# Kernel tuning notes

Hardware: AMD Instinct MI355X
Metric: run time of the kernel (lower is better)

The kernel has to match this reference:

```python
import jax, jax.numpy as jnp
import numpy as np

N_NODES = 10000
N_EDGES = 100000
C = 64          # in_channels == out_channels (required by x_i + x_m)
D_EDGE = 16     # edge_attr feature dim


def setup_inputs() -> dict:
    key = jax.random.key(0)
    k_x, k_ei, k_ea, k_w, k_b, k_r, k_bias = jax.random.split(key, 7)
    x = jax.random.normal(k_x, (N_NODES, C), dtype=jnp.float32)
    edge_index = jax.random.randint(k_ei, (2, N_EDGES), 0, N_NODES, dtype=jnp.int32)
    edge_attr = jax.random.normal(k_ea, (N_EDGES, D_EDGE), dtype=jnp.float32)
    # nn = Linear(D_EDGE -> C*C), producing per-edge [C, C] weight matrices
    W_nn = jax.random.normal(k_w, (D_EDGE, C * C), dtype=jnp.float32) * (1.0 / np.sqrt(D_EDGE))
    b_nn = jax.random.normal(k_b, (C * C,), dtype=jnp.float32) * 0.01
    root = jax.random.normal(k_r, (C, C), dtype=jnp.float32) * (1.0 / np.sqrt(C))
    bias = jax.random.normal(k_bias, (C,), dtype=jnp.float32) * 0.01
    return {"x": x, "edge_index": edge_index, "edge_attr": edge_attr,
            "W_nn": W_nn, "b_nn": b_nn, "root": root, "bias": bias}


def reference(x, edge_index, edge_attr, W_nn, b_nn, root, bias):
    N, Cc = x.shape
    row, col = edge_index[0], edge_index[1]
    # per-edge weight matrices from nn(edge_attr): [E, C, C]
    e = (edge_attr @ W_nn + b_nn).reshape(-1, Cc, Cc)
    # gather source features and apply edge-conditioned matmul: [E, C]
    m = jnp.einsum('ec,eco->eo', x[row], e)
    # Faithful to torch loop: x_m[i] = m[col == i].mean() -> SCALAR mean over
    # all elements of incoming messages, broadcast across the feature row.
    seg_sum = jax.ops.segment_sum(m.sum(axis=1), col, num_segments=N)       # [N]
    cnt = jax.ops.segment_sum(jnp.ones_like(col, dtype=x.dtype), col,
                              num_segments=N) * Cc                            # [N]
    mean = jnp.where(cnt > 0, seg_sum / jnp.maximum(cnt, 1.0), 0.0)          # [N]
    x_m = jnp.broadcast_to(mean[:, None], (N, Cc))                            # [N, C]
    # root transform + bias
    out = x @ root + bias + x_m
    return out
```

## Files before the change

### kernel.cpp

```cpp
#include <hip/hip_runtime.h>
#include <hip/hip_bf16.h>


#define CC 64
#define DE 16
#define PAD 65

__global__ __launch_bounds__(256) void k_node(const float* __restrict__ W,
                                              const float* __restrict__ b,
                                              const float* __restrict__ x,
                                              float* __restrict__ g,
                                              float* __restrict__ h,
                                              float* __restrict__ zreg,
                                              int zcount, int N) {
    __shared__ float ws[1024 + CC];
    int tid = threadIdx.x;

    for (int i = blockIdx.x * 256 + tid; i < zcount; i += gridDim.x * 256)
        zreg[i] = 0.f;

    for (int p = tid; p < 1024 + CC; p += 256) {
        const float4* src = (p < 1024) ? (const float4*)(W + (size_t)p * CC)
                                       : (const float4*)(b + (size_t)(p - 1024) * CC);
        float s = 0.f;
#pragma unroll
        for (int i = 0; i < 16; ++i) { float4 v = src[i]; s += v.x + v.y + v.z + v.w; }
        ws[p] = s;
    }
    __syncthreads();

    int n = blockIdx.x * 256 + tid;
    if (n >= N) return;

    const float4* x4  = (const float4*)(x + (size_t)n * CC);
    const float4* ws4 = (const float4*)ws;
    const float4* bs4 = (const float4*)(ws + 1024);

    float4 xr[16];
#pragma unroll
    for (int i = 0; i < 16; ++i) xr[i] = x4[i];

    float acc[DE];
#pragma unroll
    for (int d = 0; d < DE; ++d) acc[d] = 0.f;
    float hh = 0.f;

#pragma unroll
    for (int c4 = 0; c4 < 16; ++c4) {
        float4 xv = xr[c4];
        float4 bv = bs4[c4];
        hh += bv.x * xv.x + bv.y * xv.y + bv.z * xv.z + bv.w * xv.w;
#pragma unroll
        for (int d = 0; d < DE; ++d) {
            float4 wv = ws4[d * 16 + c4];
            acc[d] += wv.x * xv.x + wv.y * xv.y + wv.z * xv.z + wv.w * xv.w;
        }
    }
    float4* g4 = (float4*)(g + (size_t)n * DE);
    g4[0] = make_float4(acc[0], acc[1], acc[2], acc[3]);
    g4[1] = make_float4(acc[4], acc[5], acc[6], acc[7]);
    g4[2] = make_float4(acc[8], acc[9], acc[10], acc[11]);
    g4[3] = make_float4(acc[12], acc[13], acc[14], acc[15]);
    h[n] = hh;
}

__global__ __launch_bounds__(256) void k_edge(const int* __restrict__ ei,
                                              const float* __restrict__ ea,
                                              const float* __restrict__ g,
                                              const float* __restrict__ h,
                                              float* __restrict__ seg,
                                              float* __restrict__ cnt,
                                              int E) {
    int e = blockIdx.x * 256 + threadIdx.x;
    if (e >= E) return;
    int r  = ei[e];
    int cn = ei[E + e];
    const float4* a4 = (const float4*)(ea + (size_t)e * DE);
    const float4* g4 = (const float4*)(g + (size_t)r * DE);
    float4 a0 = a4[0], a1 = a4[1], a2 = a4[2], a3 = a4[3];
    float4 g0 = g4[0], g1 = g4[1], g2 = g4[2], g3 = g4[3];
    float s = h[r]
        + a0.x * g0.x + a0.y * g0.y + a0.z * g0.z + a0.w * g0.w
        + a1.x * g1.x + a1.y * g1.y + a1.z * g1.z + a1.w * g1.w
        + a2.x * g2.x + a2.y * g2.y + a2.z * g2.z + a2.w * g2.w
        + a3.x * g3.x + a3.y * g3.y + a3.z * g3.z + a3.w * g3.w;
    atomicAdd(seg + cn, s);
    atomicAdd(cnt + cn, 1.0f);
}

__global__ __launch_bounds__(256) void k_final(const float* __restrict__ x,
                                               const float* __restrict__ root,
                                               const float* __restrict__ bias,
                                               const float* __restrict__ seg,
                                               const float* __restrict__ cnt,
                                               float* __restrict__ out,
                                               int N) {
    __shared__ float rt[CC * CC];
    __shared__ float xs[16 * PAD];
    __shared__ float bi[CC];
    __shared__ float mn[16];
    int tid = threadIdx.x;
    int n0 = blockIdx.x * 16;

#pragma unroll
    for (int i = 0; i < 16; ++i) rt[tid + i * 256] = root[tid + i * 256];
#pragma unroll
    for (int it = 0; it < 4; ++it) {
        int i = it * 256 + tid;
        if ((size_t)n0 * CC + i < (size_t)N * CC)
            xs[(i >> 6) * PAD + (i & 63)] = x[(size_t)n0 * CC + i];
    }
    if (tid < CC) bi[tid] = bias[tid];
    if (tid < 16 && n0 + tid < N) {
        float c = cnt[n0 + tid];
        mn[tid] = c > 0.f ? seg[n0 + tid] / (c * (float)CC) : 0.f;
    }
    __syncthreads();

    int nl = tid >> 4, ci = tid & 15;
    int n = n0 + nl;
    if (n >= N) return;

    const float4* rt4 = (const float4*)rt;
    const float4* bi4 = (const float4*)bi;
    float m = mn[nl];
    float4 bv = bi4[ci];
    float4 acc = make_float4(bv.x + m, bv.y + m, bv.z + m, bv.w + m);
#pragma unroll
    for (int k = 0; k < CC; ++k) {
        float a  = xs[nl * PAD + k];
        float4 w = rt4[k * 16 + ci];
        acc.x += a * w.x; acc.y += a * w.y; acc.z += a * w.z; acc.w += a * w.w;
    }
    *(float4*)(out + (size_t)n * CC + ci * 4) = acc;
}

extern "C" void kernel_launch(void* const* d_in, const int* in_sizes, int n_in,
                              void* d_out, int out_size, void* d_ws, size_t ws_size,
                              hipStream_t stream) {
    const float* x    = (const float*)d_in[0];
    const int*   ei   = (const int*)  d_in[1];
    const float* ea   = (const float*)d_in[2];
    const float* W    = (const float*)d_in[3];
    const float* b    = (const float*)d_in[4];
    const float* root = (const float*)d_in[5];
    const float* bias = (const float*)d_in[6];
    float* out = (float*)d_out;
    float* ws  = (float*)d_ws;

    const int N = in_sizes[0] / CC;
    const int E = in_sizes[1] / 2;

    float* h    = ws;
    float* seg  = ws + N;
    float* cnt  = ws + 2 * N;
    float* g    = ws + 3 * N;

    int nBlocks = (N + 255) / 256;
    int eBlocks = (E + 255) / 256;
    int fBlocks = (N + 15) / 16;

    k_node <<<nBlocks, 256, 0, stream>>>(W, b, x, g, h, seg, 2 * N, N);
    k_edge <<<eBlocks, 256, 0, stream>>>(ei, ea, g, h, seg, cnt, E);
    k_final<<<fBlocks, 256, 0, stream>>>(x, root, bias, seg, cnt, out, N);
}
```

Baseline: 107.0 us.

## Fuse node, edge and final stages into one cooperative kernel with grid syncs

Replaces the three separate launches (node projection, edge scatter-add, root transform) with a single persistent cooperative kernel. The stages are separated by grid-wide synchronisation, and each block loops over its chunks of nodes and edges. The intent is to remove the launch gaps and tail effects between the three small kernels. In exchange it pays for two grid.sync barriers, extra host-side occupancy queries, and a persistent grid sized by occupancy. The original three-kernel path is kept as a fallback if the cooperative launch fails.

```diff
diff --git a/kernel.cpp b/kernel.cpp
--- a/kernel.cpp
+++ b/kernel.cpp
@@ -1,10 +1,133 @@
 #include <hip/hip_runtime.h>
+#include <hip/hip_cooperative_groups.h>
 #include <hip/hip_bf16.h>
+
+namespace cg = cooperative_groups;
 
 
 #define CC 64
 #define DE 16
 #define PAD 65
+
+__global__ __launch_bounds__(256) void k_fused(
+    const float* __restrict__ W, const float* __restrict__ b,
+    const float* __restrict__ x, const int* __restrict__ ei,
+    const float* __restrict__ ea, const float* __restrict__ root,
+    const float* __restrict__ bias, float* __restrict__ out,
+    float* __restrict__ g, float* __restrict__ h,
+    float* __restrict__ seg, float* __restrict__ cnt, int N, int E)
+{
+    cg::grid_group grid = cg::this_grid();
+    __shared__ float smem[CC * CC + 16 * PAD + CC + 16];
+    const int tid = threadIdx.x, bid = blockIdx.x, nb = gridDim.x;
+    const int gtid = bid * 256 + tid, gsz = nb * 256;
+
+    for (int i = gtid; i < 2 * N; i += gsz) seg[i] = 0.f;
+
+    const int nChunks = (N + 255) >> 8;
+    for (int chunk = bid; chunk < nChunks; chunk += nb) {
+        if (chunk == bid) {
+            for (int p = tid; p < 1024 + CC; p += 256) {
+                const float4* src = (p < 1024)
+                    ? (const float4*)(W + (size_t)p * CC)
+                    : (const float4*)(b + (size_t)(p - 1024) * CC);
+                float s = 0.f;
+#pragma unroll
+                for (int i = 0; i < 16; ++i) { float4 v = src[i]; s += v.x + v.y + v.z + v.w; }
+                smem[p] = s;
+            }
+            __syncthreads();
+        }
+        int n = chunk * 256 + tid;
+        if (n < N) {
+            const float4* x4  = (const float4*)(x + (size_t)n * CC);
+            const float4* ws4 = (const float4*)smem;
+            const float4* bs4 = (const float4*)(smem + 1024);
+            float4 xr[16];
+#pragma unroll
+            for (int i = 0; i < 16; ++i) xr[i] = x4[i];
+            float acc[DE];
+#pragma unroll
+            for (int d = 0; d < DE; ++d) acc[d] = 0.f;
+            float hh = 0.f;
+#pragma unroll
+            for (int c4 = 0; c4 < 16; ++c4) {
+                float4 xv = xr[c4];
+                float4 bv = bs4[c4];
+                hh += bv.x * xv.x + bv.y * xv.y + bv.z * xv.z + bv.w * xv.w;
+#pragma unroll
+                for (int d = 0; d < DE; ++d) {
+                    float4 wv = ws4[d * 16 + c4];
+                    acc[d] += wv.x * xv.x + wv.y * xv.y + wv.z * xv.z + wv.w * xv.w;
+                }
+            }
+            float4* g4 = (float4*)(g + (size_t)n * DE);
+            g4[0] = make_float4(acc[0], acc[1], acc[2], acc[3]);
+            g4[1] = make_float4(acc[4], acc[5], acc[6], acc[7]);
+            g4[2] = make_float4(acc[8], acc[9], acc[10], acc[11]);
+            g4[3] = make_float4(acc[12], acc[13], acc[14], acc[15]);
+            h[n] = hh;
+        }
+    }
+    grid.sync();
+
+    for (int e = gtid; e < E; e += gsz) {
+        int r  = ei[e];
+        int cn = ei[E + e];
+        const float4* a4 = (const float4*)(ea + (size_t)e * DE);
+        const float4* g4 = (const float4*)(g + (size_t)r * DE);
+        float4 a0 = a4[0], a1 = a4[1], a2 = a4[2], a3 = a4[3];
+        float4 g0 = g4[0], g1 = g4[1], g2 = g4[2], g3 = g4[3];
+        float s = h[r]
+            + a0.x * g0.x + a0.y * g0.y + a0.z * g0.z + a0.w * g0.w
+            + a1.x * g1.x + a1.y * g1.y + a1.z * g1.z + a1.w * g1.w
+            + a2.x * g2.x + a2.y * g2.y + a2.z * g2.z + a2.w * g2.w
+            + a3.x * g3.x + a3.y * g3.y + a3.z * g3.z + a3.w * g3.w;
+        atomicAdd(seg + cn, s);
+        atomicAdd(cnt + cn, 1.0f);
+    }
+    grid.sync();
+
+    float* rt = smem;
+    float* xs = smem + CC * CC;
+    float* bi = xs + 16 * PAD;
+    float* mn = bi + CC;
+    for (int i = tid; i < CC * CC; i += 256) rt[i] = root[i];
+    if (tid < CC) bi[tid] = bias[tid];
+
+    const int fChunks = (N + 15) >> 4;
+    for (int t = bid; t < fChunks; t += nb) {
+        int n0 = t * 16;
+        __syncthreads();
+#pragma unroll
+        for (int it = 0; it < 4; ++it) {
+            int i = it * 256 + tid;
+            if ((size_t)n0 * CC + i < (size_t)N * CC)
+                xs[(i >> 6) * PAD + (i & 63)] = x[(size_t)n0 * CC + i];
+        }
+        if (tid < 16 && n0 + tid < N) {
+            float c = cnt[n0 + tid];
+            mn[tid] = c > 0.f ? seg[n0 + tid] / (c * (float)CC) : 0.f;
+        }
+        __syncthreads();
+        int nl = tid >> 4, ci = tid & 15;
+        int n = n0 + nl;
+        if (n < N) {
+            const float4* rt4 = (const float4*)rt;
+            const float4* bi4 = (const float4*)bi;
+            float m = mn[nl];
+            float4 bv = bi4[ci];
+            float4 acc = make_float4(bv.x + m, bv.y + m, bv.z + m, bv.w + m);
+#pragma unroll
+            for (int k = 0; k < CC; ++k) {
+                float a  = xs[nl * PAD + k];
+                float4 w = rt4[k * 16 + ci];
+                acc.x += a * w.x; acc.y += a * w.y; acc.z += a * w.z; acc.w += a * w.w;
+            }
+            *(float4*)(out + (size_t)n * CC + ci * 4) = acc;
+        }
+    }
+}
 
 __global__ __launch_bounds__(256) void k_node(const float* __restrict__ W,
                                               const float* __restrict__ b,
@@ -15,10 +138,8 @@
                                               int zcount, int N) {
     __shared__ float ws[1024 + CC];
     int tid = threadIdx.x;
-
     for (int i = blockIdx.x * 256 + tid; i < zcount; i += gridDim.x * 256)
         zreg[i] = 0.f;
-
     for (int p = tid; p < 1024 + CC; p += 256) {
         const float4* src = (p < 1024) ? (const float4*)(W + (size_t)p * CC)
                                        : (const float4*)(b + (size_t)(p - 1024) * CC);
@@ -28,23 +149,18 @@
         ws[p] = s;
     }
     __syncthreads();
-
     int n = blockIdx.x * 256 + tid;
     if (n >= N) return;
-
     const float4* x4  = (const float4*)(x + (size_t)n * CC);
     const float4* ws4 = (const float4*)ws;
     const float4* bs4 = (const float4*)(ws + 1024);
-
     float4 xr[16];
 #pragma unroll
     for (int i = 0; i < 16; ++i) xr[i] = x4[i];
-
     float acc[DE];
 #pragma unroll
     for (int d = 0; d < DE; ++d) acc[d] = 0.f;
     float hh = 0.f;
-
 #pragma unroll
     for (int c4 = 0; c4 < 16; ++c4) {
         float4 xv = xr[c4];
@@ -101,7 +217,6 @@
     __shared__ float mn[16];
     int tid = threadIdx.x;
     int n0 = blockIdx.x * 16;
-
 #pragma unroll
     for (int i = 0; i < 16; ++i) rt[tid + i * 256] = root[tid + i * 256];
 #pragma unroll
@@ -116,11 +231,9 @@
         mn[tid] = c > 0.f ? seg[n0 + tid] / (c * (float)CC) : 0.f;
     }
     __syncthreads();
-
     int nl = tid >> 4, ci = tid & 15;
     int n = n0 + nl;
     if (n >= N) return;
-
     const float4* rt4 = (const float4*)rt;
     const float4* bi4 = (const float4*)bi;
     float m = mn[nl];
@@ -148,19 +261,36 @@
     float* out = (float*)d_out;
     float* ws  = (float*)d_ws;
 
-    const int N = in_sizes[0] / CC;
-    const int E = in_sizes[1] / 2;
-
-    float* h    = ws;
-    float* seg  = ws + N;
-    float* cnt  = ws + 2 * N;
-    float* g    = ws + 3 * N;
-
-    int nBlocks = (N + 255) / 256;
-    int eBlocks = (E + 255) / 256;
-    int fBlocks = (N + 15) / 16;
-
-    k_node <<<nBlocks, 256, 0, stream>>>(W, b, x, g, h, seg, 2 * N, N);
-    k_edge <<<eBlocks, 256, 0, stream>>>(ei, ea, g, h, seg, cnt, E);
-    k_final<<<fBlocks, 256, 0, stream>>>(x, root, bias, seg, cnt, out, N);
-}
+    int N = in_sizes[0] / CC;
+    int E = in_sizes[1] / 2;
+
+    float* h   = ws;
+    float* seg = ws + N;
+    float* cnt = ws + 2 * N;
+    float* g   = ws + 3 * N;
+
+    int dev = 0;
+    hipGetDevice(&dev);
+    int numCU = 256;
+    hipDeviceGetAttribute(&numCU, hipDeviceAttributeMultiprocessorCount, dev);
+    int occ = 0;
+    hipOccupancyMaxActiveBlocksPerMultiprocessor(&occ, k_fused, 256, 0);
+    if (occ < 1) occ = 1;
+    int fChunks = (N + 15) / 16;
+    int grid = occ * numCU;
+    if (grid > fChunks) grid = fChunks;
+    if (grid < 1) grid = 1;
+
+    void* args[] = { &W, &b, &x, &ei, &ea, &root, &bias, &out,
+                     &g, &h, &seg, &cnt, &N, &E };
+    hipError_t err = hipLaunchCooperativeKernel((const void*)k_fused,
+                                                dim3(grid), dim3(256),
+                                                args, 0u, stream);
+    if (err != hipSuccess) {
+        int nBlocks = (N + 255) / 256;
+        int eBlocks = (E + 255) / 256;
+        k_node <<<nBlocks, 256, 0, stream>>>(W, b, x, g, h, seg, 2 * N, N);
+        k_edge <<<eBlocks, 256, 0, stream>>>(ei, ea, g, h, seg, cnt, E);
+        k_final<<<fChunks, 256, 0, stream>>>(x, root, bias, seg, cnt, out, N);
+    }
+}
```

New measurement: 176.8 us. +65.2%, slower.
